# Performance work log

Measured on AMD Instinct MI355X. Metric: run time of the kernel, lower is better.

## Reference

```python
import jax, jax.numpy as jnp
import numpy as np
from jax import lax

B, S, M, D, NQ = 128, 100, 50, 128, 10000


def _xavier(key, shape):
    fan_in, fan_out = shape[0], shape[-1]
    limit = float(np.sqrt(6.0 / (fan_in + fan_out)))
    return jax.random.uniform(key, shape, jnp.float32, -limit, limit)


def setup_inputs() -> dict:
    key = jax.random.key(0)
    ks = jax.random.split(key, 16)
    return {
        "question_seq": jax.random.randint(ks[0], (B, S), 0, NQ),
        "answer_seq": jax.random.randint(ks[1], (B, S), 0, 2),
        "emb": _xavier(ks[2], (NQ, D)),
        "key_matrix": _xavier(ks[3], (M, D)),
        "vu_w1": _xavier(ks[4], (2 * D, D)),
        "vu_b1": jnp.zeros((D,), jnp.float32),
        "vu_w2": _xavier(ks[5], (D, D)),
        "vu_b2": jnp.zeros((D,), jnp.float32),
        "er_w": _xavier(ks[6], (D, D)),
        "er_b": jnp.zeros((D,), jnp.float32),
        "ad_w": _xavier(ks[7], (D, D)),
        "ad_b": jnp.zeros((D,), jnp.float32),
        "out_w1": _xavier(ks[8], (2 * D, D)),
        "out_b1": jnp.zeros((D,), jnp.float32),
        "out_w2": _xavier(ks[9], (D, 1)),
        "out_b2": jnp.zeros((1,), jnp.float32),
    }


def reference(question_seq, answer_seq, emb, key_matrix,
              vu_w1, vu_b1, vu_w2, vu_b2,
              er_w, er_b, ad_w, ad_b,
              out_w1, out_b1, out_w2, out_b2):
    # q_embed for all steps: [B,S,D]; attention over memory slots: [B,S,M]
    q_emb = emb[question_seq]
    attn = jax.nn.softmax(jnp.einsum('bsd,md->bsm', q_emb, key_matrix), axis=-1)

    def step(v, inp):
        w, qe = inp                                   # w: [B,M], qe: [B,D]
        read = jnp.einsum('bm,bmd->bd', w, v)         # attention read
        u = jnp.concatenate([read, qe], axis=-1)      # [B,2D]
        h = jnp.tanh(u @ vu_w1 + vu_b1)
        up = h @ vu_w2 + vu_b2                        # update vector [B,D]
        e = jax.nn.sigmoid(up @ er_w + er_b)          # erase gate
        a = jnp.tanh(up @ ad_w + ad_b)                # add vector
        v = v * (1.0 - w[:, :, None] * e[:, None, :]) + w[:, :, None] * a[:, None, :]
        return v, None

    v0 = jnp.zeros((B, M, D), q_emb.dtype)
    vT, _ = lax.scan(step, v0, (attn.transpose(1, 0, 2), q_emb.transpose(1, 0, 2)))

    # predict with last question (target_question=None branch)
    last_qe = q_emb[:, -1]                            # [B,D]
    last_w = attn[:, -1]                              # [B,M]
    read = jnp.einsum('bm,bmd->bd', last_w, vT)
    p_in = jnp.concatenate([read, last_qe], axis=-1)
    h = jax.nn.relu(p_in @ out_w1 + out_b1)
    pred = jax.nn.sigmoid(h @ out_w2 + out_b2)[:, 0]  # [B]
    return pred
```

## Files before the change

### kernel.cpp

```cpp
#include <hip/hip_runtime.h>

#define BB 128
#define SS 100
#define MM 50
#define DD 128
#define KROW 66

typedef float f32x2 __attribute__((ext_vector_type(2)));

#if defined(__has_builtin)
#  if __has_builtin(__builtin_elementwise_fma)
#    define HAVE_PKFMA 1
#  endif
#  if __has_builtin(__builtin_amdgcn_update_dpp)
#    define HAVE_DPP 1
#  endif
#endif

__device__ __forceinline__ f32x2 pkfma(f32x2 a, f32x2 b, f32x2 c) {
#ifdef HAVE_PKFMA
    return __builtin_elementwise_fma(a, b, c);
#else
    f32x2 r; r.x = fmaf(a.x, b.x, c.x); r.y = fmaf(a.y, b.y, c.y); return r;
#endif
}

__device__ __forceinline__ float qbf_add(float x) {
#ifdef HAVE_DPP
    union { float f; int i; } c, o;
    c.f = x;
    o.i = __builtin_amdgcn_update_dpp(0, c.i, 0xB1, 0xF, 0xF, true);
    x += o.f;
    c.f = x;
    o.i = __builtin_amdgcn_update_dpp(0, c.i, 0x4E, 0xF, 0xF, true);
    return x + o.f;
#else
    x += __shfl_xor(x, 1);
    x += __shfl_xor(x, 2);
    return x;
#endif
}

__device__ __forceinline__ float bf2f(unsigned short u) {
    union { unsigned int i; float f; } c; c.i = ((unsigned int)u) << 16; return c.f;
}
__device__ __forceinline__ float bfu_lo(unsigned int u) {
    union { unsigned int i; float f; } c; c.i = u << 16; return c.f;
}
__device__ __forceinline__ float bfu_hi(unsigned int u) {
    union { unsigned int i; float f; } c; c.i = u & 0xffff0000u; return c.f;
}
__device__ __forceinline__ unsigned short f2bf_bits(float f) {
    union { float f; unsigned int u; } c; c.f = f;
    unsigned int r = (c.u + 0x7FFFu + ((c.u >> 16) & 1u)) >> 16;
    return (unsigned short)r;
}
__device__ __forceinline__ unsigned int packbf(float lo, float hi) {
    return (unsigned int)f2bf_bits(lo) | ((unsigned int)f2bf_bits(hi) << 16);
}
__device__ __forceinline__ float fast_sigmoid(float x) { return 1.0f / (1.0f + __expf(-x)); }
__device__ __forceinline__ float fast_tanh(float x) {
    float ax = fabsf(x);
    float z = __expf(-2.0f * ax);
    float r = (1.0f - z) / (1.0f + z);
    return copysignf(r, x);
}

template <bool BF16>
__device__ __forceinline__ float ldw(const void* p, size_t idx) {
    if (BF16) return bf2f(((const unsigned short*)p)[idx]);
    return ((const float*)p)[idx];
}

__device__ __forceinline__ bool detect_bf16(const void* emb) {
    const unsigned int* eu = (const unsigned int*)emb;
    int cnt = 0;
    for (int i = 0; i < 32; ++i) {
        unsigned int e8 = (eu[i] >> 7) & 0xFFu;
        cnt += (e8 >= 100u && e8 <= 127u) ? 1 : 0;
    }
    return cnt >= 16;
}

#define W2ROW(r) ((r) * 68 + (((r) >> 5) << 3))

#define WS_WROW_OFF 0u
#define WS_QP_OFF   (BB * SS * 32u * 4u)
#define WS_W2EA_OFF (WS_QP_OFF + BB * SS * DD * 2u)
#define WS_EAB_OFF  (WS_W2EA_OFF + DD * DD * 8u)
#define WS_NEED     (WS_EAB_OFF + DD * 8u)

struct __align__(16) SmemA {
    union {
        struct {
            unsigned int key_w[MM * KROW];
            unsigned int qe8[8][68];
        } pre;
        unsigned int w2s[8724];
    } u;
};

template <bool BF16>
__device__ void pre_impl(const int* qseq, const void* emb, const void* key,
                         const void* vu_w1, unsigned int* wrow_g, unsigned short* qp_g,
                         SmemA& sm)
{
    const int t = threadIdx.x;
    const int b = blockIdx.x;
    const int half = blockIdx.y;
    const int l = t & 63;
    const int wv = t >> 6;
    const int q = l & 3;
    const int d = (wv << 4) + (l >> 2);

    if (BF16) {
        const unsigned int* kg = (const unsigned int*)key;
        for (int g = t; g < MM * 64; g += 512)
            sm.u.pre.key_w[(g >> 6) * KROW + (g & 63)] = kg[g];
    } else {
        const float* kf = (const float*)key;
        for (int g = t; g < MM * 64; g += 512) {
            int row = g >> 6, c2 = g & 63;
            sm.u.pre.key_w[row * KROW + c2] = packbf(kf[row * 128 + 2 * c2], kf[row * 128 + 2 * c2 + 1]);
        }
    }

    float rw1b[32];
#pragma unroll
    for (int i = 0; i < 32; ++i)
        rw1b[i] = ldw<BF16>(vu_w1, (size_t)(DD + 32 * q + i) * DD + d);
    __syncthreads();

    for (int ii = 0; ii < 7; ++ii) {
        const int nrows = (ii == 6) ? 2 : 8;
        {
            int r = t >> 6, w = t & 63;
            if (r < nrows) {
                int s = 50 * half + 8 * ii + r;
                int row = qseq[b * SS + s];
                if (BF16) {
                    sm.u.pre.qe8[r][w] = ((const unsigned int*)emb)[((size_t)row << 6) + w];
                } else {
                    const float* ef = (const float*)emb + (((size_t)row) << 7) + 2 * w;
                    sm.u.pre.qe8[r][w] = packbf(ef[0], ef[1]);
                }
            }
        }
        __syncthreads();

        if (wv < nrows) {
            int m = l;
            int mc = (m < MM) ? m : (MM - 1);
            float a0 = 0.f, a1 = 0.f, a2 = 0.f, a3 = 0.f;
#pragma unroll
            for (int j = 0; j < 32; ++j) {
                uint2 kw = *(const uint2*)&sm.u.pre.key_w[mc * KROW + 2 * j];
                uint2 qw = *(const uint2*)&sm.u.pre.qe8[wv][2 * j];
                a0 = fmaf(bfu_lo(kw.x), bfu_lo(qw.x), a0);
                a1 = fmaf(bfu_hi(kw.x), bfu_hi(qw.x), a1);
                a2 = fmaf(bfu_lo(kw.y), bfu_lo(qw.y), a2);
                a3 = fmaf(bfu_hi(kw.y), bfu_hi(qw.y), a3);
            }
            float lg = (a0 + a1) + (a2 + a3);
            if (m >= MM) lg = -1e30f;
            float mx = lg;
#pragma unroll
            for (int o = 32; o > 0; o >>= 1) mx = fmaxf(mx, __shfl_xor(mx, o));
            float p = (m < MM) ? __expf(lg - mx) : 0.f;
            float sum = p;
#pragma unroll
            for (int o = 32; o > 0; o >>= 1) sum += __shfl_xor(sum, o);
            p = p / sum;
            float pn = __shfl_xor(p, 4);
            int s = 50 * half + 8 * ii + wv;
            if ((m & 4) == 0)
                wrow_g[(size_t)(b * SS + s) * 32 + (m & 3) * 8 + (m >> 3)] = packbf(p, pn);
        }

        for (int sr = 0; sr < nrows; ++sr) {
            float p0 = 0.f, p1 = 0.f;
#pragma unroll
            for (int i = 0; i < 16; ++i) {
                unsigned int uw = sm.u.pre.qe8[sr][16 * q + i];
                p0 = fmaf(rw1b[2 * i],     bfu_lo(uw), p0);
                p1 = fmaf(rw1b[2 * i + 1], bfu_hi(uw), p1);
            }
            float qpv = qbf_add(p0 + p1);
            int s = 50 * half + 8 * ii + sr;
            if (q == 0) qp_g[(size_t)(b * SS + s) * DD + d] = f2bf_bits(qpv);
        }
        __syncthreads();
    }
}

template <bool BF16>
__device__ void build_impl(const void* vu_w2, const void* vu_b2,
                           const void* er_w, const void* er_b,
                           const void* ad_w, const void* ad_b,
                           f32x2* w2ea_g, f32x2* eab_g, SmemA& sm)
{
    const int t = threadIdx.x;
    const int l = t & 63;
    const int wv = t >> 6;
    const int q = l & 3;
    const int d = (wv << 4) + (l >> 2);

    if (BF16) {
        const unsigned int* wg = (const unsigned int*)vu_w2;
        for (int g = t; g < 128 * 64; g += 512)
            sm.u.w2s[W2ROW(g >> 6) + (g & 63)] = wg[g];
    } else {
        const float* wf = (const float*)vu_w2;
        for (int g = t; g < 128 * 64; g += 512) {
            int row = g >> 6, c2 = g & 63;
            sm.u.w2s[W2ROW(row) + c2] = packbf(wf[row * 128 + 2 * c2], wf[row * 128 + 2 * c2 + 1]);
        }
    }
    __syncthreads();

    f32x2 rw2ea[32];
#pragma unroll
    for (int k = 0; k < 32; ++k) { rw2ea[k].x = 0.f; rw2ea[k].y = 0.f; }
    f32x2 eab2; eab2.x = 0.f; eab2.y = 0.f;
#pragma unroll 1
    for (int jc = 0; jc < 4; ++jc) {
        f32x2 ea[32];
#pragma unroll
        for (int i = 0; i < 32; ++i) {
            int j = 32 * jc + i;
            ea[i].x = ldw<BF16>(er_w, (size_t)j * DD + d);
            ea[i].y = ldw<BF16>(ad_w, (size_t)j * DD + d);
            float b2j = ldw<BF16>(vu_b2, j);
            f32x2 bs; bs.x = b2j; bs.y = b2j;
            eab2 = pkfma(bs, ea[i], eab2);
        }
#pragma unroll
        for (int k = 0; k < 32; ++k) {
            const uint4* wp = (const uint4*)&sm.u.w2s[W2ROW(32 * q + k) + 16 * jc];
            uint4 A = wp[0], B = wp[1], C = wp[2], Dv = wp[3];
            unsigned int W[16] = { A.x, A.y, A.z, A.w, B.x, B.y, B.z, B.w,
                                   C.x, C.y, C.z, C.w, Dv.x, Dv.y, Dv.z, Dv.w };
            f32x2 acc = rw2ea[k];
#pragma unroll
            for (int wd = 0; wd < 16; ++wd) {
                float wlo = bfu_lo(W[wd]), whi = bfu_hi(W[wd]);
                f32x2 s0; s0.x = wlo; s0.y = wlo;
                f32x2 s1; s1.x = whi; s1.y = whi;
                acc = pkfma(s0, ea[2 * wd], acc);
                acc = pkfma(s1, ea[2 * wd + 1], acc);
            }
            rw2ea[k] = acc;
        }
    }
    eab2.x += ldw<BF16>(er_b, d);
    eab2.y += ldw<BF16>(ad_b, d);

#pragma unroll
    for (int k = 0; k < 32; ++k)
        w2ea_g[(size_t)(32 * q + k) * DD + d] = rw2ea[k];
    if (q == 0) eab_g[d] = eab2;
}

__global__ __launch_bounds__(512) void DKVMN_78546361909953_pre(
    const int* __restrict__ qseq,
    const void* emb, const void* key, const void* vu_w1,
    const void* vu_w2, const void* vu_b2,
    const void* er_w, const void* er_b, const void* ad_w, const void* ad_b,
    void* ws)
{
    __shared__ SmemA sm;
    unsigned int*   wrow_g = (unsigned int*)((char*)ws + WS_WROW_OFF);
    unsigned short* qp_g   = (unsigned short*)((char*)ws + WS_QP_OFF);
    f32x2*          w2ea_g = (f32x2*)((char*)ws + WS_W2EA_OFF);
    f32x2*          eab_g  = (f32x2*)((char*)ws + WS_EAB_OFF);
    bool isbf = detect_bf16(emb);
    if (blockIdx.x < BB) {
        if (isbf) pre_impl<true>(qseq, emb, key, vu_w1, wrow_g, qp_g, sm);
        else      pre_impl<false>(qseq, emb, key, vu_w1, wrow_g, qp_g, sm);
    } else if (blockIdx.y == 0) {
        if (isbf) build_impl<true>(vu_w2, vu_b2, er_w, er_b, ad_w, ad_b, w2ea_g, eab_g, sm);
        else      build_impl<false>(vu_w2, vu_b2, er_w, er_b, ad_w, ad_b, w2ea_g, eab_g, sm);
    }
}

struct __align__(16) SmemB {
    float xread[152];
    float xhdup[312];
    float h1f[DD];
    float qlast[DD];
};

template <bool BF16>
__device__ void scan_impl(
    const int* __restrict__ qseq,
    const void* emb, const void* vu_w1, const void* vu_b1,
    const void* out_w1, const void* out_b1, const void* out_w2, const void* out_b2,
    const unsigned int* wrow_g, const unsigned short* qp_g,
    const f32x2* w2ea_g, const f32x2* eab_g,
    void* outp, SmemB& sm)
{
    const int t = threadIdx.x;
    const int b = blockIdx.x;
    const int l = t & 63;
    const int q = l & 3;
    const int d = ((t >> 6) << 4) + (l >> 2);

    if (t < 64) {
        int row = qseq[b * SS + (SS - 1)];
        if (BF16) {
            unsigned int uw = ((const unsigned int*)emb)[((size_t)row << 6) + t];
            sm.qlast[2 * t]     = bfu_lo(uw);
            sm.qlast[2 * t + 1] = bfu_hi(uw);
        } else {
            const float* ef = (const float*)emb + (((size_t)row) << 7) + 2 * t;
            sm.qlast[2 * t]     = ef[0];
            sm.qlast[2 * t + 1] = ef[1];
        }
    }

    f32x2 rw1a2[16];
#pragma unroll
    for (int i = 0; i < 16; ++i) {
        int k0 = 32 * q + 2 * i;
        rw1a2[i].x = ldw<BF16>(vu_w1, (size_t)k0 * DD + d);
        rw1a2[i].y = ldw<BF16>(vu_w1, (size_t)(k0 + 1) * DD + d);
    }
    const float b1r = ldw<BF16>(vu_b1, d);

    f32x2 rw2ea[32];
#pragma unroll
    for (int k = 0; k < 32; ++k)
        rw2ea[k] = w2ea_g[(size_t)(32 * q + k) * DD + d];
    const f32x2 eab2 = eab_g[d];

    f32x2 v2[7];
#pragma unroll
    for (int p = 0; p < 7; ++p) { v2[p].x = 0.f; v2[p].y = 0.f; }
    f32x2 wr2[7];
    {
        const size_t r0 = (size_t)(b * SS) * 32 + q * 8;
        uint4 w0 = *(const uint4*)&wrow_g[r0];
        uint4 w1 = *(const uint4*)&wrow_g[r0 + 4];
        unsigned int ww[8] = { w0.x, w0.y, w0.z, w0.w, w1.x, w1.y, w1.z, w1.w };
#pragma unroll
        for (int p = 0; p < 7; ++p) { wr2[p].x = bfu_lo(ww[p]); wr2[p].y = bfu_hi(ww[p]); }
    }
    unsigned short qpcur = qp_g[(size_t)(b * SS) * DD + d];

    if (t < 152) sm.xread[t] = 0.f;
    __syncthreads();

    for (int s = 0; s < SS; ++s) {
        uint4 pwA, pwB;
        unsigned short pq = 0;
        const bool hasnext = (s + 1 < SS);
        if (hasnext) {
            size_t r1 = (size_t)(b * SS + s + 1);
            pwA = *(const uint4*)&wrow_g[r1 * 32 + q * 8];
            pwB = *(const uint4*)&wrow_g[r1 * 32 + q * 8 + 4];
            pq  = qp_g[r1 * DD + d];
        }

        {
            float qpv = bf2f(qpcur);
            const float4* xp = (const float4*)&sm.xread[40 * q];
            f32x2 acc2; acc2.x = 0.f; acc2.y = 0.f;
#pragma unroll
            for (int j = 0; j < 8; ++j) {
                float4 X = xp[j];
                f32x2 x01; x01.x = X.x; x01.y = X.y;
                f32x2 x23; x23.x = X.z; x23.y = X.w;
                acc2 = pkfma(rw1a2[2 * j], x01, acc2);
                acc2 = pkfma(rw1a2[2 * j + 1], x23, acc2);
            }
            float acc = qbf_add(acc2.x + acc2.y);
            float hh = fast_tanh(acc + qpv + b1r);
            if (q == 0) {
                f32x2 hd; hd.x = hh; hd.y = hh;
                *(f32x2*)&sm.xhdup[2 * d + 8 * ((2 * d) >> 5)] = hd;
            }
        }
        __syncthreads();

        {
            f32x2 acc2; acc2.x = 0.f; acc2.y = 0.f;
#pragma unroll
            for (int blk = 0; blk < 2; ++blk) {
                const float4* xp = (const float4*)&sm.xhdup[80 * q + 40 * blk];
#pragma unroll
                for (int j = 0; j < 8; ++j) {
                    float4 X = xp[j];
                    f32x2 s0; s0.x = X.x; s0.y = X.y;
                    f32x2 s1; s1.x = X.z; s1.y = X.w;
                    int k = 16 * blk + 2 * j;
                    acc2 = pkfma(rw2ea[k], s0, acc2);
                    acc2 = pkfma(rw2ea[k + 1], s1, acc2);
                }
            }
            float ae = qbf_add(acc2.x);
            float aa = qbf_add(acc2.y);
            float e = fast_sigmoid(ae + eab2.x);
            float a = fast_tanh(aa + eab2.y);
            f32x2 me; me.x = -e; me.y = -e;
            f32x2 av; av.x = a;  av.y = a;
#pragma unroll
            for (int p = 0; p < 7; ++p)
                v2[p] = pkfma(wr2[p], pkfma(me, v2[p], av), v2[p]);
            if (hasnext) {
                unsigned int ww[8] = { pwA.x, pwA.y, pwA.z, pwA.w, pwB.x, pwB.y, pwB.z, pwB.w };
#pragma unroll
                for (int p = 0; p < 7; ++p) { wr2[p].x = bfu_lo(ww[p]); wr2[p].y = bfu_hi(ww[p]); }
                qpcur = pq;
            }
            f32x2 racc; racc.x = 0.f; racc.y = 0.f;
#pragma unroll
            for (int p = 0; p < 7; ++p)
                racc = pkfma(wr2[p], v2[p], racc);
            float rr = qbf_add(racc.x + racc.y);
            if (q == 0) sm.xread[rr == rr ? (d + 8 * (d >> 5)) : 0] = rr;
        }
        __syncthreads();
    }

    float acc = 0.f;
    {
        const float4* xp = (const float4*)&sm.xread[40 * q];
        const float4* qp4 = (const float4*)&sm.qlast[32 * q];
#pragma unroll
        for (int j = 0; j < 8; ++j) {
            float4 xv = xp[j];
            float4 qv = qp4[j];
            int k = 32 * q + 4 * j;
            acc = fmaf(ldw<BF16>(out_w1, (size_t)k * DD + d),       xv.x, acc);
            acc = fmaf(ldw<BF16>(out_w1, (size_t)(k + 1) * DD + d), xv.y, acc);
            acc = fmaf(ldw<BF16>(out_w1, (size_t)(k + 2) * DD + d), xv.z, acc);
            acc = fmaf(ldw<BF16>(out_w1, (size_t)(k + 3) * DD + d), xv.w, acc);
            acc = fmaf(ldw<BF16>(out_w1, (size_t)(DD + k) * DD + d),     qv.x, acc);
            acc = fmaf(ldw<BF16>(out_w1, (size_t)(DD + k + 1) * DD + d), qv.y, acc);
            acc = fmaf(ldw<BF16>(out_w1, (size_t)(DD + k + 2) * DD + d), qv.z, acc);
            acc = fmaf(ldw<BF16>(out_w1, (size_t)(DD + k + 3) * DD + d), qv.w, acc);
        }
    }
    acc = qbf_add(acc);
    float h1 = fmaxf(acc + ldw<BF16>(out_b1, d), 0.f);
    if (q == 0) sm.h1f[d] = h1;
    __syncthreads();

    if (t < 64) {
        float xs = fmaf(sm.h1f[t], ldw<BF16>(out_w2, t),
                        sm.h1f[64 + t] * ldw<BF16>(out_w2, 64 + t));
#pragma unroll
        for (int o = 32; o > 0; o >>= 1) xs += __shfl_xor(xs, o);
        if (t == 0) {
            float pred = fast_sigmoid(xs + ldw<BF16>(out_b2, 0));
            if (BF16) ((unsigned short*)outp)[b] = f2bf_bits(pred);
            else      ((float*)outp)[b] = pred;
        }
    }
}

__global__ __launch_bounds__(512) void DKVMN_78546361909953_scan(
    const int* __restrict__ qseq,
    const void* emb, const void* vu_w1, const void* vu_b1,
    const void* out_w1, const void* out_b1, const void* out_w2, const void* out_b2,
    void* ws, void* outp)
{
    __shared__ SmemB sm;
    const unsigned int*   wrow_g = (const unsigned int*)((char*)ws + WS_WROW_OFF);
    const unsigned short* qp_g   = (const unsigned short*)((char*)ws + WS_QP_OFF);
    const f32x2*          w2ea_g = (const f32x2*)((char*)ws + WS_W2EA_OFF);
    const f32x2*          eab_g  = (const f32x2*)((char*)ws + WS_EAB_OFF);
    if (detect_bf16(emb))
        scan_impl<true>(qseq, emb, vu_w1, vu_b1, out_w1, out_b1, out_w2, out_b2,
                        wrow_g, qp_g, w2ea_g, eab_g, outp, sm);
    else
        scan_impl<false>(qseq, emb, vu_w1, vu_b1, out_w1, out_b1, out_w2, out_b2,
                         wrow_g, qp_g, w2ea_g, eab_g, outp, sm);
}

struct __align__(16) SmemM {
    union {
        struct {
            unsigned int key_w[MM * KROW];
            unsigned int qe8[8][68];
        } pre;
        struct {
            float xread[152];
            float xhdup[312];
            float h1f[DD];
        } run;
    } u;
    union {
        unsigned int w2s[8724];
        struct {
            unsigned int wrow_p[SS][32];
            unsigned short qp_all[SS][DD];
        } tab;
    } v2;
    int qrow[SS];
    float qlast[DD];
};

template <bool BF16>
__device__ void mono_impl(
    const int* __restrict__ qseq,
    const void* emb, const void* key,
    const void* vu_w1, const void* vu_b1, const void* vu_w2, const void* vu_b2,
    const void* er_w, const void* er_b, const void* ad_w, const void* ad_b,
    const void* out_w1, const void* out_b1, const void* out_w2, const void* out_b2,
    void* outp, SmemM& sm)
{
    const int t = threadIdx.x;
    const int b = blockIdx.x;
    const int l = t & 63;
    const int wv = t >> 6;
    const int q = l & 3;
    const int d = (wv << 4) + (l >> 2);

    if (BF16) {
        const unsigned int* kg = (const unsigned int*)key;
        for (int g = t; g < MM * 64; g += 512)
            sm.u.pre.key_w[(g >> 6) * KROW + (g & 63)] = kg[g];
        const unsigned int* wg = (const unsigned int*)vu_w2;
        for (int g = t; g < 128 * 64; g += 512)
            sm.v2.w2s[W2ROW(g >> 6) + (g & 63)] = wg[g];
    } else {
        const float* kf = (const float*)key;
        for (int g = t; g < MM * 64; g += 512) {
            int row = g >> 6, c2 = g & 63;
            sm.u.pre.key_w[row * KROW + c2] = packbf(kf[row * 128 + 2 * c2], kf[row * 128 + 2 * c2 + 1]);
        }
        const float* wf = (const float*)vu_w2;
        for (int g = t; g < 128 * 64; g += 512) {
            int row = g >> 6, c2 = g & 63;
            sm.v2.w2s[W2ROW(row) + c2] = packbf(wf[row * 128 + 2 * c2], wf[row * 128 + 2 * c2 + 1]);
        }
    }
    for (int g = t; g < SS; g += 512) sm.qrow[g] = qseq[b * SS + g];
    __syncthreads();

    f32x2 rw2ea[32];
#pragma unroll
    for (int k = 0; k < 32; ++k) { rw2ea[k].x = 0.f; rw2ea[k].y = 0.f; }
    f32x2 eab2; eab2.x = 0.f; eab2.y = 0.f;
#pragma unroll 1
    for (int jc = 0; jc < 4; ++jc) {
        f32x2 ea[32];
#pragma unroll
        for (int i = 0; i < 32; ++i) {
            int j = 32 * jc + i;
            ea[i].x = ldw<BF16>(er_w, (size_t)j * DD + d);
            ea[i].y = ldw<BF16>(ad_w, (size_t)j * DD + d);
            float b2j = ldw<BF16>(vu_b2, j);
            f32x2 bs; bs.x = b2j; bs.y = b2j;
            eab2 = pkfma(bs, ea[i], eab2);
        }
#pragma unroll
        for (int k = 0; k < 32; ++k) {
            const uint4* wp = (const uint4*)&sm.v2.w2s[W2ROW(32 * q + k) + 16 * jc];
            uint4 A = wp[0], B = wp[1], C = wp[2], Dv = wp[3];
            unsigned int W[16] = { A.x, A.y, A.z, A.w, B.x, B.y, B.z, B.w,
                                   C.x, C.y, C.z, C.w, Dv.x, Dv.y, Dv.z, Dv.w };
            f32x2 acc = rw2ea[k];
#pragma unroll
            for (int wd = 0; wd < 16; ++wd) {
                float wlo = bfu_lo(W[wd]), whi = bfu_hi(W[wd]);
                f32x2 s0; s0.x = wlo; s0.y = wlo;
                f32x2 s1; s1.x = whi; s1.y = whi;
                acc = pkfma(s0, ea[2 * wd], acc);
                acc = pkfma(s1, ea[2 * wd + 1], acc);
            }
            rw2ea[k] = acc;
        }
    }
    eab2.x += ldw<BF16>(er_b, d);
    eab2.y += ldw<BF16>(ad_b, d);
    __syncthreads();

    float rw1a[32], rw1b[32];
#pragma unroll
    for (int i = 0; i < 32; ++i) {
        rw1a[i] = ldw<BF16>(vu_w1, (size_t)(32 * q + i) * DD + d);
        rw1b[i] = ldw<BF16>(vu_w1, (size_t)(DD + 32 * q + i) * DD + d);
    }
    const float b1r = ldw<BF16>(vu_b1, d);

    for (int ii = 0; ii < 13; ++ii) {
        const int nrows = (ii == 12) ? 4 : 8;
        {
            int r = t >> 6, w = t & 63;
            if (r < nrows) {
                int row = sm.qrow[8 * ii + r];
                if (BF16) {
                    sm.u.pre.qe8[r][w] = ((const unsigned int*)emb)[((size_t)row << 6) + w];
                } else {
                    const float* ef = (const float*)emb + (((size_t)row) << 7) + 2 * w;
                    sm.u.pre.qe8[r][w] = packbf(ef[0], ef[1]);
                }
            }
        }
        __syncthreads();

        if (wv < nrows) {
            int m = l;
            int mc = (m < MM) ? m : (MM - 1);
            float a0 = 0.f, a1 = 0.f, a2 = 0.f, a3 = 0.f;
#pragma unroll
            for (int j = 0; j < 32; ++j) {
                uint2 kw = *(const uint2*)&sm.u.pre.key_w[mc * KROW + 2 * j];
                uint2 qw = *(const uint2*)&sm.u.pre.qe8[wv][2 * j];
                a0 = fmaf(bfu_lo(kw.x), bfu_lo(qw.x), a0);
                a1 = fmaf(bfu_hi(kw.x), bfu_hi(qw.x), a1);
                a2 = fmaf(bfu_lo(kw.y), bfu_lo(qw.y), a2);
                a3 = fmaf(bfu_hi(kw.y), bfu_hi(qw.y), a3);
            }
            float lg = (a0 + a1) + (a2 + a3);
            if (m >= MM) lg = -1e30f;
            float mx = lg;
#pragma unroll
            for (int o = 32; o > 0; o >>= 1) mx = fmaxf(mx, __shfl_xor(mx, o));
            float p = (m < MM) ? __expf(lg - mx) : 0.f;
            float sum = p;
#pragma unroll
            for (int o = 32; o > 0; o >>= 1) sum += __shfl_xor(sum, o);
            p = p / sum;
            float pn = __shfl_xor(p, 4);
            if ((m & 4) == 0)
                sm.v2.tab.wrow_p[8 * ii + wv][(m & 3) * 8 + (m >> 3)] = packbf(p, pn);
        }

        for (int sr = 0; sr < nrows; ++sr) {
            float p0 = 0.f, p1 = 0.f;
#pragma unroll
            for (int i = 0; i < 16; ++i) {
                unsigned int uw = sm.u.pre.qe8[sr][16 * q + i];
                p0 = fmaf(rw1b[2 * i],     bfu_lo(uw), p0);
                p1 = fmaf(rw1b[2 * i + 1], bfu_hi(uw), p1);
            }
            float qpv = qbf_add(p0 + p1);
            if (q == 0) sm.v2.tab.qp_all[8 * ii + sr][d] = f2bf_bits(qpv);
        }
        __syncthreads();
    }

    if (t < 64) {
        unsigned int uw = sm.u.pre.qe8[3][t];
        sm.qlast[2 * t]     = bfu_lo(uw);
        sm.qlast[2 * t + 1] = bfu_hi(uw);
    }
    f32x2 v2[7];
#pragma unroll
    for (int p = 0; p < 7; ++p) { v2[p].x = 0.f; v2[p].y = 0.f; }
    f32x2 wr2[7];
    {
        const uint4* wp = (const uint4*)&sm.v2.tab.wrow_p[0][q * 8];
        uint4 w0 = wp[0], w1 = wp[1];
        unsigned int ww[8] = { w0.x, w0.y, w0.z, w0.w, w1.x, w1.y, w1.z, w1.w };
#pragma unroll
        for (int p = 0; p < 7; ++p) { wr2[p].x = bfu_lo(ww[p]); wr2[p].y = bfu_hi(ww[p]); }
    }
    if (t < 152) sm.u.run.xread[t] = 0.f;
    __syncthreads();

    for (int s = 0; s < SS; ++s) {
        {
            float qpv = bf2f(sm.v2.tab.qp_all[s][d]);
            const float4* xp = (const float4*)&sm.u.run.xread[40 * q];
            f32x2 rw1a2_j;
            f32x2 acc2; acc2.x = 0.f; acc2.y = 0.f;
#pragma unroll
            for (int j = 0; j < 8; ++j) {
                float4 X = xp[j];
                f32x2 x01; x01.x = X.x; x01.y = X.y;
                f32x2 x23; x23.x = X.z; x23.y = X.w;
                rw1a2_j.x = rw1a[4 * j];     rw1a2_j.y = rw1a[4 * j + 1];
                acc2 = pkfma(rw1a2_j, x01, acc2);
                rw1a2_j.x = rw1a[4 * j + 2]; rw1a2_j.y = rw1a[4 * j + 3];
                acc2 = pkfma(rw1a2_j, x23, acc2);
            }
            float acc = qbf_add(acc2.x + acc2.y);
            float hh = fast_tanh(acc + qpv + b1r);
            if (q == 0) {
                f32x2 hd; hd.x = hh; hd.y = hh;
                *(f32x2*)&sm.u.run.xhdup[2 * d + 8 * ((2 * d) >> 5)] = hd;
            }
        }
        __syncthreads();

        {
            f32x2 acc2; acc2.x = 0.f; acc2.y = 0.f;
#pragma unroll
            for (int blk = 0; blk < 2; ++blk) {
                const float4* xp = (const float4*)&sm.u.run.xhdup[80 * q + 40 * blk];
#pragma unroll
                for (int j = 0; j < 8; ++j) {
                    float4 X = xp[j];
                    f32x2 s0; s0.x = X.x; s0.y = X.y;
                    f32x2 s1; s1.x = X.z; s1.y = X.w;
                    int k = 16 * blk + 2 * j;
                    acc2 = pkfma(rw2ea[k], s0, acc2);
                    acc2 = pkfma(rw2ea[k + 1], s1, acc2);
                }
            }
            float ae = qbf_add(acc2.x);
            float aa = qbf_add(acc2.y);
            float e = fast_sigmoid(ae + eab2.x);
            float a = fast_tanh(aa + eab2.y);
            f32x2 me; me.x = -e; me.y = -e;
            f32x2 av; av.x = a;  av.y = a;
#pragma unroll
            for (int p = 0; p < 7; ++p)
                v2[p] = pkfma(wr2[p], pkfma(me, v2[p], av), v2[p]);
            if (s + 1 < SS) {
                const uint4* wp = (const uint4*)&sm.v2.tab.wrow_p[s + 1][q * 8];
                uint4 w0 = wp[0], w1 = wp[1];
                unsigned int ww[8] = { w0.x, w0.y, w0.z, w0.w, w1.x, w1.y, w1.z, w1.w };
#pragma unroll
                for (int p = 0; p < 7; ++p) { wr2[p].x = bfu_lo(ww[p]); wr2[p].y = bfu_hi(ww[p]); }
            }
            f32x2 racc; racc.x = 0.f; racc.y = 0.f;
#pragma unroll
            for (int p = 0; p < 7; ++p)
                racc = pkfma(wr2[p], v2[p], racc);
            float rr = qbf_add(racc.x + racc.y);
            if (q == 0) sm.u.run.xread[d + 8 * (d >> 5)] = rr;
        }
        __syncthreads();
    }

    float acc = 0.f;
    {
        const float4* xp = (const float4*)&sm.u.run.xread[40 * q];
        const float4* qp4 = (const float4*)&sm.qlast[32 * q];
#pragma unroll
        for (int j = 0; j < 8; ++j) {
            float4 xv = xp[j];
            float4 qv = qp4[j];
            int k = 32 * q + 4 * j;
            acc = fmaf(ldw<BF16>(out_w1, (size_t)k * DD + d),       xv.x, acc);
            acc = fmaf(ldw<BF16>(out_w1, (size_t)(k + 1) * DD + d), xv.y, acc);
            acc = fmaf(ldw<BF16>(out_w1, (size_t)(k + 2) * DD + d), xv.z, acc);
            acc = fmaf(ldw<BF16>(out_w1, (size_t)(k + 3) * DD + d), xv.w, acc);
            acc = fmaf(ldw<BF16>(out_w1, (size_t)(DD + k) * DD + d),     qv.x, acc);
            acc = fmaf(ldw<BF16>(out_w1, (size_t)(DD + k + 1) * DD + d), qv.y, acc);
            acc = fmaf(ldw<BF16>(out_w1, (size_t)(DD + k + 2) * DD + d), qv.z, acc);
            acc = fmaf(ldw<BF16>(out_w1, (size_t)(DD + k + 3) * DD + d), qv.w, acc);
        }
    }
    acc = qbf_add(acc);
    float h1 = fmaxf(acc + ldw<BF16>(out_b1, d), 0.f);
    if (q == 0) sm.u.run.h1f[d] = h1;
    __syncthreads();

    if (t < 64) {
        float xs = fmaf(sm.u.run.h1f[t], ldw<BF16>(out_w2, t),
                        sm.u.run.h1f[64 + t] * ldw<BF16>(out_w2, 64 + t));
#pragma unroll
        for (int o = 32; o > 0; o >>= 1) xs += __shfl_xor(xs, o);
        if (t == 0) {
            float pred = fast_sigmoid(xs + ldw<BF16>(out_b2, 0));
            if (BF16) ((unsigned short*)outp)[b] = f2bf_bits(pred);
            else      ((float*)outp)[b] = pred;
        }
    }
}

__global__ __launch_bounds__(512) void DKVMN_78546361909953_kernel(
    const int* __restrict__ qseq,
    const void* emb, const void* key,
    const void* vu_w1, const void* vu_b1, const void* vu_w2, const void* vu_b2,
    const void* er_w, const void* er_b, const void* ad_w, const void* ad_b,
    const void* out_w1, const void* out_b1, const void* out_w2, const void* out_b2,
    void* outp)
{
    __shared__ SmemM sm;
    if (detect_bf16(emb))
        mono_impl<true>(qseq, emb, key, vu_w1, vu_b1, vu_w2, vu_b2,
                        er_w, er_b, ad_w, ad_b, out_w1, out_b1, out_w2, out_b2, outp, sm);
    else
        mono_impl<false>(qseq, emb, key, vu_w1, vu_b1, vu_w2, vu_b2,
                         er_w, er_b, ad_w, ad_b, out_w1, out_b1, out_w2, out_b2, outp, sm);
}

extern "C" void kernel_launch(void* const* d_in, const int* in_sizes, int n_in,
                              void* d_out, int out_size, void* d_ws, size_t ws_size,
                              hipStream_t stream) {
    const int* qseq = (const int*)d_in[0];
    if (ws_size >= (size_t)WS_NEED) {
        DKVMN_78546361909953_pre<<<dim3(BB + 1, 2), 512, 0, stream>>>(
            qseq, d_in[2], d_in[3], d_in[4],
            d_in[6], d_in[7], d_in[8], d_in[9], d_in[10], d_in[11], d_ws);
        DKVMN_78546361909953_scan<<<BB, 512, 0, stream>>>(
            qseq, d_in[2], d_in[4], d_in[5],
            d_in[12], d_in[13], d_in[14], d_in[15], d_ws, d_out);
    } else {
        DKVMN_78546361909953_kernel<<<BB, 512, 0, stream>>>(
            qseq, d_in[2], d_in[3], d_in[4], d_in[5], d_in[6], d_in[7],
            d_in[8], d_in[9], d_in[10], d_in[11],
            d_in[12], d_in[13], d_in[14], d_in[15], d_out);
    }
}
```

Baseline: 257.5 us.

## Split erase/add weights, drop duplicated h buffer, add ILP accumulators and lighter barriers

The erase and add weight pairs are de-interleaved into separate register arrays. This lets the second matvec read a compact, non-duplicated h vector from shared memory, halving the LDS reads per step. The single accumulation chains are split into two independent accumulators to shorten the FMA dependency chains in the serial per-step loop. __syncthreads is replaced with an explicit lgkmcnt wait, s_barrier and sched_barrier. The summation order changes slightly, and the hand-written barrier relies on only LDS traffic needing to be fenced.

```diff
diff --git a/kernel.cpp b/kernel.cpp
--- a/kernel.cpp
+++ b/kernel.cpp
@@ -39,6 +39,12 @@
     x += __shfl_xor(x, 2);
     return x;
 #endif
+}
+
+__device__ __forceinline__ void barrier_lgkm() {
+    asm volatile("s_waitcnt lgkmcnt(0)" ::: "memory");
+    __builtin_amdgcn_s_barrier();
+    __builtin_amdgcn_sched_barrier(0);
 }
 
 __device__ __forceinline__ float bf2f(unsigned short u) {
@@ -285,7 +291,7 @@
 
 struct __align__(16) SmemB {
     float xread[152];
-    float xhdup[312];
+    float xh[152];
     float h1f[DD];
     float qlast[DD];
 };
@@ -327,10 +333,14 @@
     }
     const float b1r = ldw<BF16>(vu_b1, d);
 
-    f32x2 rw2ea[32];
-#pragma unroll
-    for (int k = 0; k < 32; ++k)
-        rw2ea[k] = w2ea_g[(size_t)(32 * q + k) * DD + d];
+    f32x2 rwe2[16], rwa2[16];
+#pragma unroll
+    for (int i = 0; i < 16; ++i) {
+        f32x2 w0 = w2ea_g[(size_t)(32 * q + 2 * i) * DD + d];
+        f32x2 w1 = w2ea_g[(size_t)(32 * q + 2 * i + 1) * DD + d];
+        rwe2[i].x = w0.x; rwe2[i].y = w1.x;
+        rwa2[i].x = w0.y; rwa2[i].y = w1.y;
+    }
     const f32x2 eab2 = eab_g[d];
 
     f32x2 v2[7];
@@ -362,43 +372,42 @@
         }
 
         {
-            float qpv = bf2f(qpcur);
+            float hb = bf2f(qpcur) + b1r;
             const float4* xp = (const float4*)&sm.xread[40 * q];
-            f32x2 acc2; acc2.x = 0.f; acc2.y = 0.f;
+            f32x2 accA; accA.x = 0.f; accA.y = 0.f;
+            f32x2 accB; accB.x = 0.f; accB.y = 0.f;
 #pragma unroll
             for (int j = 0; j < 8; ++j) {
                 float4 X = xp[j];
                 f32x2 x01; x01.x = X.x; x01.y = X.y;
                 f32x2 x23; x23.x = X.z; x23.y = X.w;
-                acc2 = pkfma(rw1a2[2 * j], x01, acc2);
-                acc2 = pkfma(rw1a2[2 * j + 1], x23, acc2);
-            }
-            float acc = qbf_add(acc2.x + acc2.y);
-            float hh = fast_tanh(acc + qpv + b1r);
-            if (q == 0) {
-                f32x2 hd; hd.x = hh; hd.y = hh;
-                *(f32x2*)&sm.xhdup[2 * d + 8 * ((2 * d) >> 5)] = hd;
-            }
-        }
-        __syncthreads();
+                accA = pkfma(rw1a2[2 * j],     x01, accA);
+                accB = pkfma(rw1a2[2 * j + 1], x23, accB);
+            }
+            float acc = qbf_add((accA.x + accB.x) + (accA.y + accB.y));
+            float hh = fast_tanh(acc + hb);
+            if (q == 0) sm.xh[d + 8 * (d >> 5)] = hh;
+        }
+        barrier_lgkm();
 
         {
-            f32x2 acc2; acc2.x = 0.f; acc2.y = 0.f;
-#pragma unroll
-            for (int blk = 0; blk < 2; ++blk) {
-                const float4* xp = (const float4*)&sm.xhdup[80 * q + 40 * blk];
-#pragma unroll
-                for (int j = 0; j < 8; ++j) {
-                    float4 X = xp[j];
-                    f32x2 s0; s0.x = X.x; s0.y = X.y;
-                    f32x2 s1; s1.x = X.z; s1.y = X.w;
-                    int k = 16 * blk + 2 * j;
-                    acc2 = pkfma(rw2ea[k], s0, acc2);
-                    acc2 = pkfma(rw2ea[k + 1], s1, acc2);
-                }
-            }
-            float ae = qbf_add(acc2.x);
-            float aa = qbf_add(acc2.y);
+            const float4* xp = (const float4*)&sm.xh[40 * q];
+            f32x2 ae1; ae1.x = 0.f; ae1.y = 0.f;
+            f32x2 ae2; ae2.x = 0.f; ae2.y = 0.f;
+            f32x2 aa1; aa1.x = 0.f; aa1.y = 0.f;
+            f32x2 aa2; aa2.x = 0.f; aa2.y = 0.f;
+#pragma unroll
+            for (int j = 0; j < 8; ++j) {
+                float4 X = xp[j];
+                f32x2 h01; h01.x = X.x; h01.y = X.y;
+                f32x2 h23; h23.x = X.z; h23.y = X.w;
+                ae1 = pkfma(rwe2[2 * j],     h01, ae1);
+                aa1 = pkfma(rwa2[2 * j],     h01, aa1);
+                ae2 = pkfma(rwe2[2 * j + 1], h23, ae2);
+                aa2 = pkfma(rwa2[2 * j + 1], h23, aa2);
+            }
+            float ae = qbf_add((ae1.x + ae2.x) + (ae1.y + ae2.y));
+            float aa = qbf_add((aa1.x + aa2.x) + (aa1.y + aa2.y));
             float e = fast_sigmoid(ae + eab2.x);
             float a = fast_tanh(aa + eab2.y);
             f32x2 me; me.x = -e; me.y = -e;
@@ -412,14 +421,16 @@
                 for (int p = 0; p < 7; ++p) { wr2[p].x = bfu_lo(ww[p]); wr2[p].y = bfu_hi(ww[p]); }
                 qpcur = pq;
             }
-            f32x2 racc; racc.x = 0.f; racc.y = 0.f;
-#pragma unroll
-            for (int p = 0; p < 7; ++p)
-                racc = pkfma(wr2[p], v2[p], racc);
-            float rr = qbf_add(racc.x + racc.y);
+            f32x2 rA; rA.x = 0.f; rA.y = 0.f;
+            f32x2 rB; rB.x = 0.f; rB.y = 0.f;
+            rA = pkfma(wr2[0], v2[0], rA); rB = pkfma(wr2[1], v2[1], rB);
+            rA = pkfma(wr2[2], v2[2], rA); rB = pkfma(wr2[3], v2[3], rB);
+            rA = pkfma(wr2[4], v2[4], rA); rB = pkfma(wr2[5], v2[5], rB);
+            rA = pkfma(wr2[6], v2[6], rA);
+            float rr = qbf_add((rA.x + rB.x) + (rA.y + rB.y));
             if (q == 0) sm.xread[rr == rr ? (d + 8 * (d >> 5)) : 0] = rr;
         }
-        __syncthreads();
+        barrier_lgkm();
     }
 
     float acc = 0.f;
```

Result: faster. 251.9 us (-2.2%).
